# Kernel optimization log

Hardware: AMD Instinct MI355X
Metric: run time of the kernel (lower is better)

## Reference

```python
import jax, jax.numpy as jnp
import numpy as np
import math

B, T, D = 2, 2048, 1024
H, HD = 16, 64
E, TOPK, HID = 8, 2, 2048
EPS = 1e-6


def setup_inputs() -> dict:
    key = jax.random.key(0)
    ks = jax.random.split(key, 12)
    s = 0.02
    # RoPE freqs: [T, HD//2, 2] (cos, sin)
    inv = 1.0 / (10000.0 ** (np.arange(0, HD, 2, dtype=np.float32) / HD))
    ang = np.outer(np.arange(T, dtype=np.float32), inv)  # [T, HD//2]
    freqs_cis = jnp.asarray(np.stack([np.cos(ang), np.sin(ang)], axis=-1))
    # causal additive mask [T, T]
    mask = jnp.where(jnp.tril(jnp.ones((T, T), dtype=bool)), 0.0, -jnp.inf).astype(jnp.float32)
    return {
        "x": jax.random.normal(ks[0], (B, T, D), jnp.float32),
        "freqs_cis": freqs_cis,
        "mask": mask,
        "attn_norm_w": jnp.ones((D,), jnp.float32),
        "ffn_norm_w": jnp.ones((D,), jnp.float32),
        "wq": jax.random.normal(ks[1], (D, D), jnp.float32) * s,
        "wk": jax.random.normal(ks[2], (D, D), jnp.float32) * s,
        "wv": jax.random.normal(ks[3], (D, D), jnp.float32) * s,
        "wo": jax.random.normal(ks[4], (D, D), jnp.float32) * s,
        "gate_w": jax.random.normal(ks[5], (D, E), jnp.float32) * s,
        "w1": jax.random.normal(ks[6], (E, D, HID), jnp.float32) * s,
        "w2": jax.random.normal(ks[7], (E, HID, D), jnp.float32) * s,
        "w3": jax.random.normal(ks[8], (E, D, HID), jnp.float32) * s,
    }


def rmsnorm(x, w):
    rms = jax.lax.rsqrt(jnp.mean(x * x, axis=-1, keepdims=True) + EPS)
    return x * rms * w


def rope(q, fc):
    # q: [B, T, H, HD], fc: [T, HD//2, 2]
    qr = q.reshape(*q.shape[:-1], HD // 2, 2)
    cos = fc[None, :, None, :, 0]
    sin = fc[None, :, None, :, 1]
    r0 = qr[..., 0] * cos - qr[..., 1] * sin
    r1 = qr[..., 0] * sin + qr[..., 1] * cos
    return jnp.stack([r0, r1], axis=-1).reshape(q.shape)


def reference(x, freqs_cis, mask, attn_norm_w, ffn_norm_w, wq, wk, wv, wo,
              gate_w, w1, w2, w3):
    # ---- attention sub-block (pre-norm) ----
    h = rmsnorm(x, attn_norm_w)
    q = (h @ wq).reshape(B, T, H, HD)
    k = (h @ wk).reshape(B, T, H, HD)
    v = (h @ wv).reshape(B, T, H, HD)
    q = rope(q, freqs_cis)
    k = rope(k, freqs_cis)
    new_k, new_v = k, v  # kv cache (no prior cache)
    scale = 1.0 / math.sqrt(HD)
    scores = jnp.einsum("bqhd,bkhd->bhqk", q, k) * scale + mask[None, None]
    attn = jax.nn.softmax(scores, axis=-1)
    out = jnp.einsum("bhqk,bkhd->bqhd", attn, v).reshape(B, T, D)
    x = x + out @ wo

    # ---- MoE sub-block (pre-norm) ----
    hf = rmsnorm(x, ffn_norm_w).reshape(-1, D)  # [N, D]
    gate_probs = jax.nn.softmax(hf @ gate_w, axis=-1)  # [N, E]
    topk_vals, topk_idx = jax.lax.top_k(gate_probs, TOPK)
    topk_w = topk_vals / (jnp.sum(topk_vals, axis=-1, keepdims=True) + 1e-8)
    # per-token per-expert combine weight [N, E]
    comb = jnp.sum(topk_w[:, :, None] * jax.nn.one_hot(topk_idx, E), axis=1)
    # dense per-expert SwiGLU (faithful linear combination of expert outputs)
    h1 = jnp.einsum("nd,edh->enh", hf, w1)
    h3 = jnp.einsum("nd,edh->enh", hf, w3)
    y = jnp.einsum("enh,ehd->end", jax.nn.silu(h1) * h3, w2)
    moe_out = jnp.einsum("ne,end->nd", comb, y).reshape(B, T, D)
    x = x + moe_out
    return (x, new_k, new_v)
```

## Files before the change

kernel.cpp:

```cpp
#include <hip/hip_runtime.h>

#define T_SEQ   2048
#define D_MODEL 1024
#define NHEAD   16
#define NEXP    8
#define HID_DIM 2048
#define NTOK    4096
#define MAXBLK  72
#define SLOTS   9216

typedef unsigned short u16;
typedef unsigned int   u32;
typedef __bf16 bf16_t;
typedef bf16_t bf16x8 __attribute__((ext_vector_type(8)));
typedef float  f32x4  __attribute__((ext_vector_type(4)));
typedef float  f32x2  __attribute__((ext_vector_type(2)));
typedef u32    u32x4  __attribute__((ext_vector_type(4)));

typedef __attribute__((address_space(1))) const void* gptr1_t;
typedef __attribute__((address_space(3))) void*       lptr3_t;

__device__ __forceinline__ u16 f2bf_bits(float f) {
  u32 u = __builtin_bit_cast(u32, f);
  u += 0x7FFFu + ((u >> 16) & 1u);
  return (u16)(u >> 16);
}
__device__ __forceinline__ float bf2f(u16 s) {
  return __builtin_bit_cast(float, (u32)s << 16);
}
__device__ __forceinline__ bf16x8 frag_b128(const u16* p) {
  return *reinterpret_cast<const bf16x8*>(p);
}
__device__ __forceinline__ u16 cvt_bf16(float f) {
  return __builtin_bit_cast(u16, (__bf16)f);
}
#define MFMA16(a,b,c) __builtin_amdgcn_mfma_f32_16x16x32_bf16((a),(b),(c),0,0,0)

__device__ __forceinline__ void gload16(const void* g, void* l) {
  __builtin_amdgcn_global_load_lds((gptr1_t)g, (lptr3_t)l, 16, 0, 0);
}

__device__ __forceinline__ void stage128x32(const u16* gbase, size_t ldk, int kt,
                                            u16* lds, int wid, int lane) {
  int rl = lane >> 2, cc = lane & 3;
#pragma unroll
  for (int h = 0; h < 2; ++h) {
    int row = wid*32 + h*16 + rl;
    int chunk = cc ^ ((row >> 1) & 3);
    gload16(gbase + (size_t)row*ldk + kt + chunk*8, lds + (size_t)(wid*32 + h*16)*32);
  }
}
__device__ __forceinline__ bf16x8 fragLDS(const u16* lds, int row, int l4, int l15) {
  int chunk = l4 ^ ((l15 >> 1) & 3);
  return frag_b128(lds + row*32 + chunk*8);
}

__device__ __forceinline__ void stage128x64(const u16* gbase, size_t ldk, int kt,
                                            u16* lds, int wid, int lane) {
  int rl = lane >> 3, cc = lane & 7;
#pragma unroll
  for (int g = 0; g < 4; ++g) {
    int row = wid*32 + g*8 + rl;
    int chunk = cc ^ (row & 7);
    gload16(gbase + (size_t)row*ldk + kt + chunk*8, lds + (size_t)(wid*32 + g*8)*64);
  }
}
__device__ __forceinline__ void stage64x64(const u16* gbase, size_t ldk, int kt,
                                           u16* lds, int wid, int lane) {
  int rl = lane >> 3, cc = lane & 7;
#pragma unroll
  for (int g = 0; g < 2; ++g) {
    int row = wid*16 + g*8 + rl;
    int chunk = cc ^ (row & 7);
    gload16(gbase + (size_t)row*ldk + kt + chunk*8, lds + (size_t)(wid*16 + g*8)*64);
  }
}
__device__ __forceinline__ bf16x8 fragLDS64(const u16* lds, int row, int s, int l4, int l15) {
  int chunk = (s*4 + l4) ^ (l15 & 7);
  return frag_b128(lds + row*64 + chunk*8);
}

template<int SPLIT>
__global__ __launch_bounds__(256) void rmsnorm_kernel(
    const float* __restrict__ x, const float* __restrict__ w,
    u16* __restrict__ hi, u16* __restrict__ lo)
{
  int row = blockIdx.x, tid = threadIdx.x;
  const float* xr = x + (size_t)row * D_MODEL;
  f32x4 v = *reinterpret_cast<const f32x4*>(xr + tid * 4);
  float ss = v[0]*v[0] + v[1]*v[1] + v[2]*v[2] + v[3]*v[3];
#pragma unroll
  for (int off = 32; off >= 1; off >>= 1) ss += __shfl_xor(ss, off);
  __shared__ float part[4];
  if ((tid & 63) == 0) part[tid >> 6] = ss;
  __syncthreads();
  float rms = rsqrtf((part[0]+part[1]+part[2]+part[3]) * (1.0f/D_MODEL) + 1e-6f);
  f32x4 wv = *reinterpret_cast<const f32x4*>(w + tid * 4);
  u32 hw0=0, hw1=0, lw0=0, lw1=0;
#pragma unroll
  for (int j = 0; j < 4; ++j) {
    float f = v[j] * rms * wv[j];
    u16 hb = f2bf_bits(f);
    if (j < 2) hw0 |= (u32)hb << (16*j); else hw1 |= (u32)hb << (16*(j-2));
    if (SPLIT) {
      u16 lb = f2bf_bits(f - bf2f(hb));
      if (j < 2) lw0 |= (u32)lb << (16*j); else lw1 |= (u32)lb << (16*(j-2));
    }
  }
  u32* hp = reinterpret_cast<u32*>(hi + (size_t)row * D_MODEL + tid * 4);
  hp[0] = hw0; hp[1] = hw1;
  if (SPLIT) {
    u32* lp = reinterpret_cast<u32*>(lo + (size_t)row * D_MODEL + tid * 4);
    lp[0] = lw0; lp[1] = lw1;
  }
}

template<int SPLIT>
__global__ __launch_bounds__(256) void transpose_kernel(
    const float* __restrict__ src, u16* __restrict__ dhi, u16* __restrict__ dlo,
    int R, int C)
{
  __shared__ float tile[64][65];
  src += (size_t)blockIdx.z * R * C;
  dhi += (size_t)blockIdx.z * R * C;
  if (SPLIT) dlo += (size_t)blockIdx.z * R * C;
  int r0 = blockIdx.y*64, c0 = blockIdx.x*64;
  int t = threadIdx.x;
  int lr = t>>2, lc4 = (t&3)*16;
#pragma unroll
  for (int i = 0; i < 4; ++i)
    *reinterpret_cast<f32x4*>(&tile[lr][lc4 + i*4]) =
        *reinterpret_cast<const f32x4*>(src + (size_t)(r0+lr)*C + c0 + lc4 + i*4);
  __syncthreads();
#pragma unroll
  for (int h = 0; h < 2; ++h) {
    int oc = h*32 + (t>>3);
    int ok = (t&7)*8;
    union { u16 a[8]; u32x4 v; } hb, lb;
#pragma unroll
    for (int j = 0; j < 8; ++j) {
      float f = tile[ok+j][oc];
      hb.a[j] = f2bf_bits(f);
      if (SPLIT) lb.a[j] = f2bf_bits(f - bf2f(hb.a[j]));
    }
    *reinterpret_cast<u32x4*>(dhi + (size_t)(c0+oc)*R + r0 + ok) = hb.v;
    if (SPLIT)
      *reinterpret_cast<u32x4*>(dlo + (size_t)(c0+oc)*R + r0 + ok) = lb.v;
  }
}

__global__ __launch_bounds__(256) void transpose_qkv_kernel(
    const float* __restrict__ wq, const float* __restrict__ wk, const float* __restrict__ wv,
    u16* __restrict__ dhi, u16* __restrict__ dlo)
{
  __shared__ float tile[64][65];
  int z = blockIdx.z;
  const float* src = (z == 0) ? wq : ((z == 1) ? wk : wv);
  dhi += (size_t)z * D_MODEL * D_MODEL;
  dlo += (size_t)z * D_MODEL * D_MODEL;
  int r0 = blockIdx.y*64, c0 = blockIdx.x*64;
  int t = threadIdx.x;
  int lr = t>>2, lc4 = (t&3)*16;
#pragma unroll
  for (int i = 0; i < 4; ++i)
    *reinterpret_cast<f32x4*>(&tile[lr][lc4 + i*4]) =
        *reinterpret_cast<const f32x4*>(src + (size_t)(r0+lr)*D_MODEL + c0 + lc4 + i*4);
  __syncthreads();
#pragma unroll
  for (int h = 0; h < 2; ++h) {
    int oc = h*32 + (t>>3);
    int ok = (t&7)*8;
    union { u16 a[8]; u32x4 v; } hb, lb;
#pragma unroll
    for (int j = 0; j < 8; ++j) {
      float f = tile[ok+j][oc];
      hb.a[j] = f2bf_bits(f);
      lb.a[j] = f2bf_bits(f - bf2f(hb.a[j]));
    }
    *reinterpret_cast<u32x4*>(dhi + (size_t)(c0+oc)*D_MODEL + r0 + ok) = hb.v;
    *reinterpret_cast<u32x4*>(dlo + (size_t)(c0+oc)*D_MODEL + r0 + ok) = lb.v;
  }
}

__global__ __launch_bounds__(256) void v_transpose_kernel(
    const u16* __restrict__ vbf, u16* __restrict__ vT)
{
  __shared__ u16 tile[64][72];
  int bh = blockIdx.y, b = bh >> 4, h = bh & 15;
  int t0 = blockIdx.x * 64;
  int t = threadIdx.x;
  int row = t >> 2, c16 = (t & 3) * 16;
  const u16* src = vbf + ((size_t)(b*T_SEQ + t0 + row))*D_MODEL + h*64 + c16;
  *reinterpret_cast<u32x4*>(&tile[row][c16])     = *reinterpret_cast<const u32x4*>(src);
  *reinterpret_cast<u32x4*>(&tile[row][c16 + 8]) = *reinterpret_cast<const u32x4*>(src + 8);
  __syncthreads();
  int d = row, k0 = c16;
  union { u16 a[16]; u32x4 v[2]; } o;
#pragma unroll
  for (int j = 0; j < 16; ++j) o.a[j] = tile[k0 + j][d];
  u16* dst = vT + ((size_t)bh*64 + d)*T_SEQ + t0 + k0;
  *reinterpret_cast<u32x4*>(dst)     = o.v[0];
  *reinterpret_cast<u32x4*>(dst + 8) = o.v[1];
}

__global__ __launch_bounds__(256) void qkv_gemm_kernel(
    const u16* __restrict__ Ahi, const u16* __restrict__ Alo,
    const u16* __restrict__ Bhi, const u16* __restrict__ Blo,
    const float* __restrict__ freqs,
    u16* __restrict__ qhi, u16* __restrict__ qlo,
    u16* __restrict__ khi, u16* __restrict__ klo,
    u16* __restrict__ vbf, float* __restrict__ kout, float* __restrict__ vout)
{
  const int K = D_MODEL;
  __shared__ __align__(16) u16 AhS[2][128*32], AlS[2][128*32],
                               BhS[2][128*32], BlS[2][128*32];
  int tid = threadIdx.x, lane = tid & 63, wid = tid >> 6;
  int wm = wid >> 1, wn = wid & 1;
  int l15 = lane & 15, l4 = lane >> 4;
  size_t bm = (size_t)blockIdx.y * 128, bn = (size_t)blockIdx.x * 128;
  const u16* Ah0 = Ahi + bm*K;  const u16* Al0 = Alo + bm*K;
  const u16* Bh0 = Bhi + bn*K;  const u16* Bl0 = Blo + bn*K;
  f32x4 acc[4][4] = {};
  stage128x32(Ah0, K, 0, AhS[0], wid, lane);
  stage128x32(Al0, K, 0, AlS[0], wid, lane);
  stage128x32(Bh0, K, 0, BhS[0], wid, lane);
  stage128x32(Bl0, K, 0, BlS[0], wid, lane);
  __syncthreads();
  int cur = 0;
  for (int kt = 0; kt < K; kt += 32) {
    if (kt + 32 < K) {
      int nxt = cur ^ 1;
      stage128x32(Ah0, K, kt + 32, AhS[nxt], wid, lane);
      stage128x32(Al0, K, kt + 32, AlS[nxt], wid, lane);
      stage128x32(Bh0, K, kt + 32, BhS[nxt], wid, lane);
      stage128x32(Bl0, K, kt + 32, BlS[nxt], wid, lane);
    }
    bf16x8 ah[4], al[4];
#pragma unroll
    for (int mi = 0; mi < 4; ++mi) {
      int row = wm*64 + mi*16 + l15;
      ah[mi] = fragLDS(AhS[cur], row, l4, l15);
      al[mi] = fragLDS(AlS[cur], row, l4, l15);
    }
#pragma unroll
    for (int ni = 0; ni < 4; ++ni) {
      int row = wn*64 + ni*16 + l15;
      bf16x8 bh = fragLDS(BhS[cur], row, l4, l15);
      bf16x8 bl = fragLDS(BlS[cur], row, l4, l15);
#pragma unroll
      for (int mi = 0; mi < 4; ++mi) {
        acc[mi][ni] = MFMA16(ah[mi], bh, acc[mi][ni]);
        acc[mi][ni] = MFMA16(ah[mi], bl, acc[mi][ni]);
        acc[mi][ni] = MFMA16(al[mi], bh, acc[mi][ni]);
      }
    }
    __syncthreads();
    cur ^= 1;
  }
  int mat = (int)(bn >> 10);
  int colbase = (int)(bn & 1023);
  int evenl = !(lane & 1);
#pragma unroll
  for (int mi = 0; mi < 4; ++mi) {
#pragma unroll
    for (int r = 0; r < 4; ++r) {
      int tok = (int)bm + wm*64 + mi*16 + l4*4 + r;
      int t = tok & (T_SEQ - 1);
#pragma unroll
      for (int ni = 0; ni < 4; ++ni) {
        int col = colbase + wn*64 + ni*16 + l15;
        float v = acc[mi][ni][r];
        if (mat == 2) {
          float vp = __shfl_xor(v, 1);
          if (evenl) {
            u32 pk = (u32)cvt_bf16(v) | ((u32)cvt_bf16(vp) << 16);
            *reinterpret_cast<u32*>(vbf + (size_t)tok*D_MODEL + col) = pk;
            f32x2 fv; fv[0] = v; fv[1] = vp;
            *reinterpret_cast<f32x2*>(vout + (size_t)tok*D_MODEL + col) = fv;
          }
        } else {
          int d = col & 63, p = d >> 1;
          f32x2 cs = *reinterpret_cast<const f32x2*>(freqs + ((size_t)t*32 + p)*2);
          float partner = __shfl_xor(v, 1);
          float rot = (d & 1) ? (partner*cs[1] + v*cs[0]) : (v*cs[0] - partner*cs[1]);
          float rotp = __shfl_xor(rot, 1);
          if (evenl) {
            u16 h0 = cvt_bf16(rot), h1 = cvt_bf16(rotp);
            u32 hp = (u32)h0 | ((u32)h1 << 16);
            u32 lp = (u32)cvt_bf16(rot - bf2f(h0)) | ((u32)cvt_bf16(rotp - bf2f(h1)) << 16);
            if (mat == 0) {
              *reinterpret_cast<u32*>(qhi + (size_t)tok*D_MODEL + col) = hp;
              *reinterpret_cast<u32*>(qlo + (size_t)tok*D_MODEL + col) = lp;
            } else {
              *reinterpret_cast<u32*>(khi + (size_t)tok*D_MODEL + col) = hp;
              *reinterpret_cast<u32*>(klo + (size_t)tok*D_MODEL + col) = lp;
              f32x2 fv; fv[0] = rot; fv[1] = rotp;
              *reinterpret_cast<f32x2*>(kout + (size_t)tok*D_MODEL + col) = fv;
            }
          }
        }
      }
    }
  }
}

__global__ __launch_bounds__(256) void wo_gemm_kernel(
    const u16* __restrict__ A, const u16* __restrict__ Bt,
    const float* __restrict__ resid, float* __restrict__ Cout)
{
  const int K = D_MODEL, N = D_MODEL;
  __shared__ __align__(16) u16 As[128*32], Bs[128*32];
  int tid = threadIdx.x, lane = tid & 63, wid = tid >> 6;
  int wm = wid >> 1, wn = wid & 1;
  int l15 = lane & 15, l4 = lane >> 4;
  size_t bm = (size_t)blockIdx.y * 128, bn = (size_t)blockIdx.x * 128;
  const u16* A0 = A + bm*K;  const u16* B0 = Bt + bn*K;
  f32x4 acc[4][4] = {};
  for (int kt = 0; kt < K; kt += 32) {
    __syncthreads();
    stage128x32(A0, K, kt, As, wid, lane);
    stage128x32(B0, K, kt, Bs, wid, lane);
    __syncthreads();
    bf16x8 a[4];
#pragma unroll
    for (int mi = 0; mi < 4; ++mi)
      a[mi] = fragLDS(As, wm*64 + mi*16 + l15, l4, l15);
#pragma unroll
    for (int ni = 0; ni < 4; ++ni) {
      bf16x8 b = fragLDS(Bs, wn*64 + ni*16 + l15, l4, l15);
#pragma unroll
      for (int mi = 0; mi < 4; ++mi)
        acc[mi][ni] = MFMA16(a[mi], b, acc[mi][ni]);
    }
  }
#pragma unroll
  for (int mi = 0; mi < 4; ++mi)
#pragma unroll
    for (int ni = 0; ni < 4; ++ni)
#pragma unroll
      for (int r = 0; r < 4; ++r) {
        size_t row = bm + wm*64 + mi*16 + l4*4 + r;
        size_t col = bn + wn*64 + ni*16 + l15;
        Cout[row*N + col] = resid[row*N + col] + acc[mi][ni][r];
      }
}

__global__ __launch_bounds__(64) void wg2_kernel(
    const float* __restrict__ wo, const float* __restrict__ ffnw,
    const float* __restrict__ gw, float* __restrict__ wg2)
{
  int d = blockIdx.x, lane = threadIdx.x;
  const float* wr = wo + (size_t)d * D_MODEL;
  float acc[8] = {0,0,0,0,0,0,0,0};
#pragma unroll
  for (int i = 0; i < 4; ++i) {
    int c = lane*4 + i*256;
    f32x4 wv = *reinterpret_cast<const f32x4*>(wr + c);
    f32x4 fv = *reinterpret_cast<const f32x4*>(ffnw + c);
#pragma unroll
    for (int j = 0; j < 4; ++j) {
      float a = wv[j] * fv[j];
      f32x4 g0 = *reinterpret_cast<const f32x4*>(gw + (size_t)(c + j)*NEXP);
      f32x4 g1 = *reinterpret_cast<const f32x4*>(gw + (size_t)(c + j)*NEXP + 4);
      acc[0]+=a*g0[0]; acc[1]+=a*g0[1]; acc[2]+=a*g0[2]; acc[3]+=a*g0[3];
      acc[4]+=a*g1[0]; acc[5]+=a*g1[1]; acc[6]+=a*g1[2]; acc[7]+=a*g1[3];
    }
  }
#pragma unroll
  for (int off = 32; off >= 1; off >>= 1)
#pragma unroll
    for (int e = 0; e < 8; ++e) acc[e] += __shfl_xor(acc[e], off);
  if (lane == 0) {
#pragma unroll
    for (int e = 0; e < 8; ++e) wg2[(size_t)d*NEXP + e] = acc[e];
  }
}

__global__ __launch_bounds__(256) void vg_kernel(
    const float* __restrict__ vf, const float* __restrict__ wg2, float* __restrict__ Vg)
{
  int tok = blockIdx.x * 4 + (threadIdx.x >> 6);
  int lane = threadIdx.x & 63;
  int hh = lane >> 2, part = lane & 3;
  const float* vr = vf + (size_t)tok * D_MODEL + hh*64 + part*16;
  const float* gr = wg2 + (size_t)(hh*64 + part*16) * NEXP;
  float acc[8] = {0,0,0,0,0,0,0,0};
#pragma unroll
  for (int i = 0; i < 4; ++i) {
    f32x4 vv = *reinterpret_cast<const f32x4*>(vr + i*4);
#pragma unroll
    for (int j = 0; j < 4; ++j) {
      float a = vv[j];
      f32x4 g0 = *reinterpret_cast<const f32x4*>(gr + (size_t)(i*4 + j)*NEXP);
      f32x4 g1 = *reinterpret_cast<const f32x4*>(gr + (size_t)(i*4 + j)*NEXP + 4);
      acc[0]+=a*g0[0]; acc[1]+=a*g0[1]; acc[2]+=a*g0[2]; acc[3]+=a*g0[3];
      acc[4]+=a*g1[0]; acc[5]+=a*g1[1]; acc[6]+=a*g1[2]; acc[7]+=a*g1[3];
    }
  }
#pragma unroll
  for (int off = 1; off < 4; off <<= 1)
#pragma unroll
    for (int e = 0; e < 8; ++e) acc[e] += __shfl_xor(acc[e], off);
  if (part == 0) {
#pragma unroll
    for (int e = 0; e < 8; ++e) Vg[((size_t)tok*NHEAD + hh)*NEXP + e] = acc[e];
  }
}

__global__ __launch_bounds__(256) void attn_kernel(
    const u16* __restrict__ Qhi, const u16* __restrict__ Qlo,
    const u16* __restrict__ Khi, const u16* __restrict__ Klo,
    const u16* __restrict__ vT, const float* __restrict__ Vg,
    u16* __restrict__ Ob, float* __restrict__ raw_ao)
{
  int id = blockIdx.x;
  int bh = id & 31, b = bh >> 4, h = bh & 15;
  int rr_ = id >> 8, kk_ = (id >> 5) & 7;
  int qt = (rr_ == 0) ? (31 - kk_) : (rr_ == 1) ? (16 + kk_)
         : (rr_ == 2) ? (15 - kk_) : kk_;
  int tid = threadIdx.x, lane = tid & 63, wid = tid >> 6;
  int l15 = lane & 15, l4 = lane >> 4;

  __shared__ __align__(16) u16 VTs[64*64];
  __shared__ __align__(16) u16 Pl[4][16][72];
  __shared__ float VgS[64][12];
  __shared__ __align__(16) u16 KhS[64*64], KlS[64*64];

  const u16* vTb = vT + ((size_t)bh * 64) * T_SEQ;

  size_t qoff = ((size_t)(b*T_SEQ + qt*64 + wid*16)) * D_MODEL + h*64;
  bf16x8 qhiF[2], qloF[2];
#pragma unroll
  for (int s = 0; s < 2; ++s) {
    qhiF[s] = frag_b128(Qhi + qoff + (size_t)l15*D_MODEL + s*32 + l4*8);
    qloF[s] = frag_b128(Qlo + qoff + (size_t)l15*D_MODEL + s*32 + l4*8);
  }
  float m_r[4], l_r[4];
  f32x4 racc4[4][2] = {};
  f32x4 oacc[4] = {};
#pragma unroll
  for (int r = 0; r < 4; ++r) { m_r[r] = -1e30f; l_r[r] = 0.f; }

  for (int kt = 0; kt <= qt; ++kt) {
    __syncthreads();
    {
      const u16* kbH = Khi + ((size_t)(b*T_SEQ + kt*64))*D_MODEL + h*64;
      const u16* kbL = Klo + ((size_t)(b*T_SEQ + kt*64))*D_MODEL + h*64;
      stage64x64(kbH, D_MODEL, 0, KhS, wid, lane);
      stage64x64(kbL, D_MODEL, 0, KlS, wid, lane);
      stage64x64(vTb, T_SEQ, kt*64, VTs, wid, lane);
    }
    if (tid < 128) {
      int key = tid >> 1, eh = (tid & 1) * 4;
      const float* gsrc = Vg + ((size_t)(b*T_SEQ + kt*64 + key)*NHEAD + h)*NEXP + eh;
      *reinterpret_cast<f32x4*>(&VgS[key][eh]) = *reinterpret_cast<const f32x4*>(gsrc);
    }
    __syncthreads();

    f32x4 sacc[4] = {};
    __builtin_amdgcn_s_setprio(1);
#pragma unroll
    for (int n = 0; n < 4; ++n) {
#pragma unroll
      for (int s = 0; s < 2; ++s) {
        bf16x8 khiF = fragLDS64(KhS, n*16 + l15, s, l4, l15);
        bf16x8 kloF = fragLDS64(KlS, n*16 + l15, s, l4, l15);
        sacc[n] = MFMA16(qhiF[s], khiF, sacc[n]);
        sacc[n] = MFMA16(qhiF[s], kloF, sacc[n]);
        sacc[n] = MFMA16(qloF[s], khiF, sacc[n]);
      }
    }
    __builtin_amdgcn_s_setprio(0);
#pragma unroll
    for (int n = 0; n < 4; ++n)
#pragma unroll
      for (int r = 0; r < 4; ++r)
        sacc[n][r] *= 0.125f;
    if (kt == qt) {
      int q0 = qt*64 + wid*16 + l4*4;
      int k00 = kt*64 + l15;
#pragma unroll
      for (int n = 0; n < 4; ++n)
#pragma unroll
        for (int r = 0; r < 4; ++r)
          if (k00 + n*16 > q0 + r) sacc[n][r] = -1e30f;
    }
    float rm[4];
#pragma unroll
    for (int r = 0; r < 4; ++r) {
      float v = fmaxf(fmaxf(sacc[0][r], sacc[1][r]), fmaxf(sacc[2][r], sacc[3][r]));
#pragma unroll
      for (int off = 1; off < 16; off <<= 1) v = fmaxf(v, __shfl_xor(v, off));
      rm[r] = v;
    }
    int needp = (rm[0] > m_r[0]+8.f) | (rm[1] > m_r[1]+8.f) |
                (rm[2] > m_r[2]+8.f) | (rm[3] > m_r[3]+8.f);
    if (__any(needp)) {
#pragma unroll
      for (int r = 0; r < 4; ++r) {
        float mn = fmaxf(m_r[r], rm[r]);
        float corr = __expf(m_r[r] - mn);
        m_r[r] = mn;
        l_r[r] *= corr;
        racc4[r][0] *= corr; racc4[r][1] *= corr;
#pragma unroll
        for (int n = 0; n < 4; ++n) oacc[n][r] *= corr;
      }
    }
#pragma unroll
    for (int r = 0; r < 4; ++r) {
      float rs = 0.f;
#pragma unroll
      for (int n = 0; n < 4; ++n) {
        float pp = __expf(sacc[n][r] - m_r[r]);
        sacc[n][r] = pp;
        rs += pp;
      }
#pragma unroll
      for (int off = 1; off < 16; off <<= 1) rs += __shfl_xor(rs, off);
      l_r[r] += rs;
    }
#pragma unroll
    for (int n = 0; n < 4; ++n)
#pragma unroll
      for (int r = 0; r < 4; ++r)
        Pl[wid][l4*4 + r][n*16 + l15] = cvt_bf16(sacc[n][r]);
#pragma unroll
    for (int n = 0; n < 4; ++n) {
      f32x4 g0 = *reinterpret_cast<const f32x4*>(&VgS[n*16 + l15][0]);
      f32x4 g1 = *reinterpret_cast<const f32x4*>(&VgS[n*16 + l15][4]);
#pragma unroll
      for (int r = 0; r < 4; ++r) {
        float pp = sacc[n][r];
        racc4[r][0] += g0 * pp;
        racc4[r][1] += g1 * pp;
      }
    }
    __builtin_amdgcn_s_setprio(1);
#pragma unroll
    for (int s = 0; s < 2; ++s) {
      bf16x8 pa = frag_b128(&Pl[wid][l15][s*32 + l4*8]);
#pragma unroll
      for (int n = 0; n < 4; ++n) {
        bf16x8 vb8 = fragLDS64(VTs, n*16 + l15, s, l4, l15);
        oacc[n] = MFMA16(pa, vb8, oacc[n]);
      }
    }
    __builtin_amdgcn_s_setprio(0);
  }
  float inv[4];
#pragma unroll
  for (int r = 0; r < 4; ++r) inv[r] = 1.0f / l_r[r];
  size_t obase = ((size_t)(b*T_SEQ + qt*64 + wid*16))*D_MODEL + h*64;
#pragma unroll
  for (int n = 0; n < 4; ++n)
#pragma unroll
    for (int r = 0; r < 4; ++r)
      Ob[obase + (size_t)(l4*4 + r)*D_MODEL + n*16 + l15] = cvt_bf16(oacc[n][r]*inv[r]);
  float rv[4][8];
#pragma unroll
  for (int r = 0; r < 4; ++r)
#pragma unroll
    for (int e = 0; e < 8; ++e)
      rv[r][e] = (e < 4) ? racc4[r][0][e] : racc4[r][1][e-4];
#pragma unroll
  for (int off = 1; off < 16; off <<= 1)
#pragma unroll
    for (int r = 0; r < 4; ++r)
#pragma unroll
      for (int e = 0; e < 8; ++e)
        rv[r][e] += __shfl_xor(rv[r][e], off);
  if (l15 == 0) {
#pragma unroll
    for (int r = 0; r < 4; ++r) {
      size_t tokg = (size_t)(b*T_SEQ) + qt*64 + wid*16 + l4*4 + r;
#pragma unroll
      for (int e = 0; e < 8; ++e)
        raw_ao[(tokg*NHEAD + h)*NEXP + e] = rv[r][e]*inv[r];
    }
  }
}

__global__ void zero_counts_kernel(int* counts) {
  if (threadIdx.x < NEXP) counts[threadIdx.x] = 0;
}

__global__ __launch_bounds__(256) void gate2_kernel(
    const float* __restrict__ x, const float* __restrict__ x2,
    const float* __restrict__ ffnw, const float* __restrict__ gw,
    const float* __restrict__ raw_ao,
    int* __restrict__ gidx, float* __restrict__ gwt, int* __restrict__ counts)
{
  int tok = blockIdx.x * 4 + (threadIdx.x >> 6);
  int lane = threadIdx.x & 63;
  const float* xr = x + (size_t)tok * D_MODEL;
  const float* x2r = x2 + (size_t)tok * D_MODEL;
  float ss = 0.f;
  float lg[8] = {0,0,0,0,0,0,0,0};
#pragma unroll
  for (int i = 0; i < 4; ++i) {
    int d = lane*4 + i*256;
    f32x4 xv = *reinterpret_cast<const f32x4*>(xr + d);
    f32x4 x2v = *reinterpret_cast<const f32x4*>(x2r + d);
    f32x4 wv = *reinterpret_cast<const f32x4*>(ffnw + d);
    ss += x2v[0]*x2v[0] + x2v[1]*x2v[1] + x2v[2]*x2v[2] + x2v[3]*x2v[3];
#pragma unroll
    for (int j = 0; j < 4; ++j) {
      float a = xv[j]*wv[j];
      f32x4 g0 = *reinterpret_cast<const f32x4*>(gw + (size_t)(d + j)*NEXP);
      f32x4 g1 = *reinterpret_cast<const f32x4*>(gw + (size_t)(d + j)*NEXP + 4);
      lg[0]+=a*g0[0]; lg[1]+=a*g0[1]; lg[2]+=a*g0[2]; lg[3]+=a*g0[3];
      lg[4]+=a*g1[0]; lg[5]+=a*g1[1]; lg[6]+=a*g1[2]; lg[7]+=a*g1[3];
    }
  }
#pragma unroll
  for (int off = 1; off < 64; off <<= 1) {
    ss += __shfl_xor(ss, off);
#pragma unroll
    for (int e = 0; e < 8; ++e) lg[e] += __shfl_xor(lg[e], off);
  }
  float ah[8] = {0,0,0,0,0,0,0,0};
  if (lane < 16) {
    const float* ar = raw_ao + ((size_t)tok*NHEAD + lane)*NEXP;
#pragma unroll
    for (int e = 0; e < 8; ++e) ah[e] = ar[e];
  }
#pragma unroll
  for (int off = 1; off < 16; off <<= 1)
#pragma unroll
    for (int e = 0; e < 8; ++e) ah[e] += __shfl_xor(ah[e], off);
  if (lane == 0) {
    float rms = rsqrtf(ss*(1.0f/D_MODEL) + 1e-6f);
    float lo_[8], pp[8];
    float mx = -1e30f;
#pragma unroll
    for (int e = 0; e < 8; ++e) { lo_[e] = (lg[e] + ah[e]) * rms; mx = fmaxf(mx, lo_[e]); }
    float sum = 0.f;
#pragma unroll
    for (int e = 0; e < 8; ++e) { pp[e] = __expf(lo_[e] - mx); sum += pp[e]; }
    float isum = 1.0f/sum;
#pragma unroll
    for (int e = 0; e < 8; ++e) pp[e] *= isum;
    int i0 = 0;
    for (int e = 1; e < 8; ++e) if (pp[e] > pp[i0]) i0 = e;
    int i1 = (i0 == 0) ? 1 : 0;
    for (int e = 0; e < 8; ++e) if (e != i0 && pp[e] > pp[i1]) i1 = e;
    float v0 = pp[i0], v1 = pp[i1];
    float wnorm = 1.0f/(v0 + v1 + 1e-8f);
    gidx[2*tok] = i0; gidx[2*tok+1] = i1;
    gwt[2*tok] = v0*wnorm; gwt[2*tok+1] = v1*wnorm;
    atomicAdd(&counts[i0], 1); atomicAdd(&counts[i1], 1);
  }
}

__global__ __launch_bounds__(256) void scan_kernel(
    const int* __restrict__ counts, int* __restrict__ base, int* __restrict__ fill,
    int* __restrict__ blk_expert, int* __restrict__ perm_token)
{
  if (threadIdx.x == 0) {
    int b = 0, blk = 0;
    for (int e = 0; e < NEXP; ++e) {
      base[e] = b;
      fill[e] = 0;
      int nb = (counts[e] + 127) >> 7;
      for (int i = 0; i < nb; ++i) blk_expert[blk++] = e;
      b += nb << 7;
    }
    for (; blk < MAXBLK; ++blk) blk_expert[blk] = -1;
  }
  for (int i = threadIdx.x; i < SLOTS; i += 256) perm_token[i] = -1;
}

__global__ __launch_bounds__(256) void scatter_kernel(
    const int* __restrict__ gidx, const int* __restrict__ base, int* __restrict__ fill,
    int* __restrict__ perm_token, int* __restrict__ tok_slot)
{
  int t = blockIdx.x * 256 + threadIdx.x;
  if (t >= NTOK) return;
#pragma unroll
  for (int r = 0; r < 2; ++r) {
    int e = gidx[2*t + r];
    int pos = base[e] + atomicAdd(&fill[e], 1);
    perm_token[pos] = t;
    tok_slot[2*t + r] = pos;
  }
}

__global__ __launch_bounds__(256) void moe_gemm1_kernel(
    const u16* __restrict__ Ah, const u16* __restrict__ W1t, const u16* __restrict__ W3t,
    const int* __restrict__ perm_token, const int* __restrict__ blk_expert,
    u16* __restrict__ tbuf)
{
  int mb = blockIdx.y;
  int e = blk_expert[mb];
  if (e < 0) return;
  const int K = D_MODEL;
  __shared__ __align__(16) u16 As[128*64], B1s[64*64], B3s[64*64];
  int tid = threadIdx.x, lane = tid & 63, wid = tid >> 6;
  int wm = wid >> 1, wn = wid & 1;
  int l15 = lane & 15, l4 = lane >> 4;
  size_t bn = (size_t)blockIdx.x * 64;
  const u16* w1e = W1t + (size_t)e * HID_DIM * D_MODEL + bn*K;
  const u16* w3e = W3t + (size_t)e * HID_DIM * D_MODEL + bn*K;
  int rl = lane >> 3, cc = lane & 7;
  int tokA[4];
#pragma unroll
  for (int g = 0; g < 4; ++g) {
    int row = wid*32 + g*8 + rl;
    int t = perm_token[mb*128 + row];
    tokA[g] = t < 0 ? 0 : t;
  }
  f32x4 acc1[4][2] = {}, acc3[4][2] = {};
  for (int kt = 0; kt < K; kt += 64) {
    __syncthreads();
#pragma unroll
    for (int g = 0; g < 4; ++g) {
      int row = wid*32 + g*8 + rl;
      int chunk = cc ^ (row & 7);
      gload16(Ah + (size_t)tokA[g]*K + kt + chunk*8, As + (size_t)(wid*32 + g*8)*64);
    }
    stage64x64(w1e, K, kt, B1s, wid, lane);
    stage64x64(w3e, K, kt, B3s, wid, lane);
    __syncthreads();
#pragma unroll
    for (int s = 0; s < 2; ++s) {
      bf16x8 a[4];
#pragma unroll
      for (int mi = 0; mi < 4; ++mi)
        a[mi] = fragLDS64(As, wm*64 + mi*16 + l15, s, l4, l15);
#pragma unroll
      for (int ni = 0; ni < 2; ++ni) {
        int row = wn*32 + ni*16 + l15;
        bf16x8 b1 = fragLDS64(B1s, row, s, l4, l15);
        bf16x8 b3 = fragLDS64(B3s, row, s, l4, l15);
#pragma unroll
        for (int mi = 0; mi < 4; ++mi) {
          acc1[mi][ni] = MFMA16(a[mi], b1, acc1[mi][ni]);
          acc3[mi][ni] = MFMA16(a[mi], b3, acc3[mi][ni]);
        }
      }
    }
  }
  int evenl = !(lane & 1);
#pragma unroll
  for (int mi = 0; mi < 4; ++mi)
#pragma unroll
    for (int ni = 0; ni < 2; ++ni)
#pragma unroll
      for (int r = 0; r < 4; ++r) {
        size_t slot = (size_t)mb*128 + wm*64 + mi*16 + l4*4 + r;
        size_t col = bn + wn*32 + ni*16 + l15;
        float h1 = acc1[mi][ni][r], h3 = acc3[mi][ni][r];
        float t = h1 * __builtin_amdgcn_rcpf(1.0f + __expf(-h1)) * h3;
        float tp = __shfl_xor(t, 1);
        if (evenl) {
          u32 pk = (u32)cvt_bf16(t) | ((u32)cvt_bf16(tp) << 16);
          *reinterpret_cast<u32*>(tbuf + slot*HID_DIM + col) = pk;
        }
      }
}

__global__ __launch_bounds__(256) void moe_gemm2_kernel(
    const u16* __restrict__ tbuf, const u16* __restrict__ W2t,
    const int* __restrict__ blk_expert, u16* __restrict__ ybuf)
{
  int mb = blockIdx.y;
  int e = blk_expert[mb];
  if (e < 0) return;
  const int K = HID_DIM, N = D_MODEL;
  __shared__ __align__(16) u16 As[128*32], Bs[128*32];
  int tid = threadIdx.x, lane = tid & 63, wid = tid >> 6;
  int wm = wid >> 1, wn = wid & 1;
  int l15 = lane & 15, l4 = lane >> 4;
  size_t bm = (size_t)mb * 128, bn = (size_t)blockIdx.x * 128;
  const u16* A0 = tbuf + bm*K;
  const u16* B0 = W2t + (size_t)e * D_MODEL * HID_DIM + bn*K;
  f32x4 acc[4][4] = {};
  for (int kt = 0; kt < K; kt += 32) {
    __syncthreads();
    stage128x32(A0, K, kt, As, wid, lane);
    stage128x32(B0, K, kt, Bs, wid, lane);
    __syncthreads();
    bf16x8 a[4];
#pragma unroll
    for (int mi = 0; mi < 4; ++mi)
      a[mi] = fragLDS(As, wm*64 + mi*16 + l15, l4, l15);
#pragma unroll
    for (int ni = 0; ni < 4; ++ni) {
      bf16x8 b = fragLDS(Bs, wn*64 + ni*16 + l15, l4, l15);
#pragma unroll
      for (int mi = 0; mi < 4; ++mi)
        acc[mi][ni] = MFMA16(a[mi], b, acc[mi][ni]);
    }
  }
  int evenl = !(lane & 1);
#pragma unroll
  for (int mi = 0; mi < 4; ++mi)
#pragma unroll
    for (int ni = 0; ni < 4; ++ni)
#pragma unroll
      for (int r = 0; r < 4; ++r) {
        float v = acc[mi][ni][r];
        float vp = __shfl_xor(v, 1);
        if (evenl) {
          size_t slot = bm + wm*64 + mi*16 + l4*4 + r;
          size_t col = bn + wn*64 + ni*16 + l15;
          u32 pk = (u32)cvt_bf16(v) | ((u32)cvt_bf16(vp) << 16);
          *reinterpret_cast<u32*>(ybuf + slot*N + col) = pk;
        }
      }
}

__global__ __launch_bounds__(256) void combine_kernel(
    const float* __restrict__ x2, const u16* __restrict__ ybuf,
    const int* __restrict__ tok_slot, const float* __restrict__ gwt,
    float* __restrict__ xout)
{
  int t = blockIdx.x;
  int c = threadIdx.x * 4;
  int s0 = tok_slot[2*t], s1 = tok_slot[2*t+1];
  float w0 = gwt[2*t], w1 = gwt[2*t+1];
  f32x4 xv = *reinterpret_cast<const f32x4*>(x2 + (size_t)t * D_MODEL + c);
  const u16* y0 = ybuf + (size_t)s0 * D_MODEL + c;
  const u16* y1 = ybuf + (size_t)s1 * D_MODEL + c;
  f32x4 o;
#pragma unroll
  for (int j = 0; j < 4; ++j)
    o[j] = xv[j] + w0 * bf2f(y0[j]) + w1 * bf2f(y1[j]);
  *reinterpret_cast<f32x4*>(xout + (size_t)t * D_MODEL + c) = o;
}

extern "C" void kernel_launch(void* const* d_in, const int* in_sizes, int n_in,
                              void* d_out, int out_size, void* d_ws, size_t ws_size,
                              hipStream_t stream)
{
  (void)in_sizes; (void)n_in; (void)out_size; (void)ws_size;
  const float* x     = (const float*)d_in[0];
  const float* freqs = (const float*)d_in[1];
  const float* attnw = (const float*)d_in[3];
  const float* ffnw  = (const float*)d_in[4];
  const float* wq    = (const float*)d_in[5];
  const float* wk    = (const float*)d_in[6];
  const float* wv    = (const float*)d_in[7];
  const float* wo    = (const float*)d_in[8];
  const float* gw    = (const float*)d_in[9];
  const float* w1    = (const float*)d_in[10];
  const float* w2    = (const float*)d_in[11];
  const float* w3    = (const float*)d_in[12];
  float* xout = (float*)d_out;
  float* kout = xout + (size_t)NTOK * D_MODEL;
  float* vout = kout + (size_t)NTOK * D_MODEL;

  const size_t PLANE = (size_t)NTOK * D_MODEL * 2;
  const size_t QKVT  = (size_t)3 * D_MODEL * D_MODEL * 2;
  const size_t TBUFB = (size_t)SLOTS * HID_DIM * 2;
  const size_t WEXP  = (size_t)NEXP * D_MODEL * HID_DIM * 2;
  char* base = (char*)d_ws;
  u16* hhi      = (u16*)(base);
  u16* hlo      = (u16*)(base + PLANE);
  u16* wqkvT_hi = (u16*)(base + 2*PLANE);
  u16* wqkvT_lo = (u16*)(base + 2*PLANE + QKVT);
  u16* woT      = (u16*)(base + 2*PLANE);
  u16* tbuf     = (u16*)(base);
  char* Qb = base + TBUFB;
  u16* qhi = (u16*)(Qb);
  u16* qlo = (u16*)(Qb + PLANE);
  u16* khi = (u16*)(Qb + 2*PLANE);
  u16* klo = (u16*)(Qb + 3*PLANE);
  u16* vbf = (u16*)(Qb + 4*PLANE);
  u16* w1T  = (u16*)(Qb);
  u16* ybuf = (u16*)(Qb);
  char* Sb = Qb + 5*PLANE;
  u16* aobf = (u16*)(Sb);
  u16* vT   = (u16*)(Sb + PLANE);
  u16* w3T  = (u16*)(Sb);
  u16* w2T  = (u16*)(Sb);
  char* Tb = Sb + WEXP;
  u16* hf = (u16*)(Tb);
  float* x2 = (float*)(Tb + PLANE);
  char* p = Tb + PLANE + (size_t)NTOK * D_MODEL * 4;
  float* wg2    = (float*)p;  p += 32768;
  float* Vg     = (float*)p;  p += (size_t)NTOK*NHEAD*NEXP*4;
  float* raw_ao = (float*)p;  p += (size_t)NTOK*NHEAD*NEXP*4;
  int*   gidx   = (int*)p;    p += 32768;
  float* gwt    = (float*)p;  p += 32768;
  int*   tok_slot = (int*)p;  p += 32768;
  int*   perm   = (int*)p;    p += SLOTS*4;
  int*   counts = (int*)p;
  int*   base_  = counts + 8;
  int*   fill_  = counts + 16;
  int*   blk_e  = counts + 24;

  dim3 blk(256);
  rmsnorm_kernel<1><<<NTOK, blk, 0, stream>>>(x, attnw, hhi, hlo);
  wg2_kernel<<<D_MODEL, 64, 0, stream>>>(wo, ffnw, gw, wg2);
  zero_counts_kernel<<<1, 64, 0, stream>>>(counts);
  dim3 tg3(16, 16, 3);
  transpose_qkv_kernel<<<tg3, blk, 0, stream>>>(wq, wk, wv, wqkvT_hi, wqkvT_lo);
  dim3 gqkv(24, 32);
  qkv_gemm_kernel<<<gqkv, blk, 0, stream>>>(hhi, hlo, wqkvT_hi, wqkvT_lo, freqs,
                                            qhi, qlo, khi, klo, vbf, kout, vout);
  dim3 gvt(T_SEQ/64, 32);
  v_transpose_kernel<<<gvt, blk, 0, stream>>>(vbf, vT);
  dim3 tg(16, 16);
  transpose_kernel<0><<<tg, blk, 0, stream>>>(wo, woT, nullptr, D_MODEL, D_MODEL);
  vg_kernel<<<NTOK/4, blk, 0, stream>>>(vout, wg2, Vg);
  attn_kernel<<<dim3(1024), blk, 0, stream>>>(qhi, qlo, khi, klo, vT, Vg, aobf, raw_ao);
  dim3 tw13(HID_DIM/64, D_MODEL/64, NEXP);
  transpose_kernel<0><<<tw13, blk, 0, stream>>>(w1, w1T, nullptr, D_MODEL, HID_DIM);
  dim3 g88(D_MODEL/128, NTOK/128);
  wo_gemm_kernel<<<g88, blk, 0, stream>>>(aobf, woT, x, x2);
  transpose_kernel<0><<<tw13, blk, 0, stream>>>(w3, w3T, nullptr, D_MODEL, HID_DIM);
  rmsnorm_kernel<0><<<NTOK, blk, 0, stream>>>(x2, ffnw, hf, nullptr);
  gate2_kernel<<<NTOK/4, blk, 0, stream>>>(x, x2, ffnw, gw, raw_ao, gidx, gwt, counts);
  scan_kernel<<<1, blk, 0, stream>>>(counts, base_, fill_, blk_e, perm);
  scatter_kernel<<<NTOK/256, blk, 0, stream>>>(gidx, base_, fill_, perm, tok_slot);
  dim3 g1(HID_DIM/64, MAXBLK);
  moe_gemm1_kernel<<<g1, blk, 0, stream>>>(hf, w1T, w3T, perm, blk_e, tbuf);
  dim3 tw2(D_MODEL/64, HID_DIM/64, NEXP);
  transpose_kernel<0><<<tw2, blk, 0, stream>>>(w2, w2T, nullptr, HID_DIM, D_MODEL);
  dim3 g2(D_MODEL/128, MAXBLK);
  moe_gemm2_kernel<<<g2, blk, 0, stream>>>(tbuf, w2T, blk_e, ybuf);
  combine_kernel<<<NTOK, blk, 0, stream>>>(x2, ybuf, tok_slot, gwt, xout);
}
```

Before: 740.2 us.

## Widen QKV GEMM tile to 128x256 and drop LDS double buffering

The QKV projection GEMM now computes a 128x256 output tile per block, with each wave holding 4x8 accumulator fragments, and launches half as many blocks in N. This raises A-tile reuse and MFMA work per LDS fragment load. To fit LDS, the ping-pong double buffer is replaced by a single buffer with two barriers per K step, so global loads no longer overlap with compute. It also roughly doubles accumulator registers, which may lower occupancy, and the grid shrinks to 384 blocks.

```diff
diff --git a/kernel.cpp b/kernel.cpp
--- a/kernel.cpp
+++ b/kernel.cpp
@@ -212,41 +212,36 @@
     u16* __restrict__ vbf, float* __restrict__ kout, float* __restrict__ vout)
 {
   const int K = D_MODEL;
-  __shared__ __align__(16) u16 AhS[2][128*32], AlS[2][128*32],
-                               BhS[2][128*32], BlS[2][128*32];
+  __shared__ __align__(16) u16 AhS[128*32], AlS[128*32],
+                               BhS[256*32], BlS[256*32];
   int tid = threadIdx.x, lane = tid & 63, wid = tid >> 6;
   int wm = wid >> 1, wn = wid & 1;
   int l15 = lane & 15, l4 = lane >> 4;
-  size_t bm = (size_t)blockIdx.y * 128, bn = (size_t)blockIdx.x * 128;
+  size_t bm = (size_t)blockIdx.y * 128, bn = (size_t)blockIdx.x * 256;
   const u16* Ah0 = Ahi + bm*K;  const u16* Al0 = Alo + bm*K;
   const u16* Bh0 = Bhi + bn*K;  const u16* Bl0 = Blo + bn*K;
-  f32x4 acc[4][4] = {};
-  stage128x32(Ah0, K, 0, AhS[0], wid, lane);
-  stage128x32(Al0, K, 0, AlS[0], wid, lane);
-  stage128x32(Bh0, K, 0, BhS[0], wid, lane);
-  stage128x32(Bl0, K, 0, BlS[0], wid, lane);
-  __syncthreads();
-  int cur = 0;
+  f32x4 acc[4][8] = {};
   for (int kt = 0; kt < K; kt += 32) {
-    if (kt + 32 < K) {
-      int nxt = cur ^ 1;
-      stage128x32(Ah0, K, kt + 32, AhS[nxt], wid, lane);
-      stage128x32(Al0, K, kt + 32, AlS[nxt], wid, lane);
-      stage128x32(Bh0, K, kt + 32, BhS[nxt], wid, lane);
-      stage128x32(Bl0, K, kt + 32, BlS[nxt], wid, lane);
-    }
+    __syncthreads();
+    stage128x32(Ah0, K, kt, AhS, wid, lane);
+    stage128x32(Al0, K, kt, AlS, wid, lane);
+    stage128x32(Bh0, K, kt, BhS, wid, lane);
+    stage128x32(Bh0 + (size_t)128*K, K, kt, BhS + 128*32, wid, lane);
+    stage128x32(Bl0, K, kt, BlS, wid, lane);
+    stage128x32(Bl0 + (size_t)128*K, K, kt, BlS + 128*32, wid, lane);
+    __syncthreads();
     bf16x8 ah[4], al[4];
 #pragma unroll
     for (int mi = 0; mi < 4; ++mi) {
       int row = wm*64 + mi*16 + l15;
-      ah[mi] = fragLDS(AhS[cur], row, l4, l15);
-      al[mi] = fragLDS(AlS[cur], row, l4, l15);
-    }
-#pragma unroll
-    for (int ni = 0; ni < 4; ++ni) {
-      int row = wn*64 + ni*16 + l15;
-      bf16x8 bh = fragLDS(BhS[cur], row, l4, l15);
-      bf16x8 bl = fragLDS(BlS[cur], row, l4, l15);
+      ah[mi] = fragLDS(AhS, row, l4, l15);
+      al[mi] = fragLDS(AlS, row, l4, l15);
+    }
+#pragma unroll
+    for (int ni = 0; ni < 8; ++ni) {
+      int row = wn*128 + ni*16 + l15;
+      bf16x8 bh = fragLDS(BhS, row, l4, l15);
+      bf16x8 bl = fragLDS(BlS, row, l4, l15);
 #pragma unroll
       for (int mi = 0; mi < 4; ++mi) {
         acc[mi][ni] = MFMA16(ah[mi], bh, acc[mi][ni]);
@@ -254,8 +249,6 @@
         acc[mi][ni] = MFMA16(al[mi], bh, acc[mi][ni]);
       }
     }
-    __syncthreads();
-    cur ^= 1;
   }
   int mat = (int)(bn >> 10);
   int colbase = (int)(bn & 1023);
@@ -267,8 +260,8 @@
       int tok = (int)bm + wm*64 + mi*16 + l4*4 + r;
       int t = tok & (T_SEQ - 1);
 #pragma unroll
-      for (int ni = 0; ni < 4; ++ni) {
-        int col = colbase + wn*64 + ni*16 + l15;
+      for (int ni = 0; ni < 8; ++ni) {
+        int col = colbase + wn*128 + ni*16 + l15;
         float v = acc[mi][ni][r];
         if (mat == 2) {
           float vp = __shfl_xor(v, 1);
@@ -897,7 +890,7 @@
   zero_counts_kernel<<<1, 64, 0, stream>>>(counts);
   dim3 tg3(16, 16, 3);
   transpose_qkv_kernel<<<tg3, blk, 0, stream>>>(wq, wk, wv, wqkvT_hi, wqkvT_lo);
-  dim3 gqkv(24, 32);
+  dim3 gqkv(12, 32);
   qkv_gemm_kernel<<<gqkv, blk, 0, stream>>>(hhi, hlo, wqkvT_hi, wqkvT_lo, freqs,
                                             qhi, qlo, khi, klo, vbf, kout, vout);
   dim3 gvt(T_SEQ/64, 32);
```

Result: slower. 869.3 us (+17.4%).
